# Kernel optimization log

Measured on AMD Instinct MI355X. Metric: run time of the kernel, lower is better.

The kernel has to match this reference:

```python
import jax, jax.numpy as jnp
import numpy as np

NEIGHB = 16   # k neighbors
GROUP = 32    # GroupNorm groups (== outc/2 -> per-channel instance norm)
EPS = 1e-5


def _lrelu(x, slope):
    return jnp.where(x >= 0, x, slope * x)


def _gn(x, gamma, beta, groups=GROUP, eps=EPS):
    # GroupNorm over [B, C, S, K]
    B, C, S, K = x.shape
    xr = x.reshape(B, groups, (C // groups) * S * K)
    m = xr.mean(-1, keepdims=True)
    v = xr.var(-1, keepdims=True)
    xn = ((xr - m) * jax.lax.rsqrt(v + eps)).reshape(B, C, S, K)
    return xn * gamma[None, :, None, None] + beta[None, :, None, None]


def _sample(x, rand_num, s_num, k):
    # Dynamic_sampling.forward, s_num <= P branch (s_num == P here)
    B, C, P = x.shape
    perm = jnp.argsort(rand_num, axis=1)[:, :s_num]                    # [B,S]
    sel = jnp.take_along_axis(x, perm[:, None, :], axis=2)             # [B,C,S]
    x3, s3 = x[:, :3], sel[:, :3]
    # pairwise = -||xi - qj||^2, shape [B,P,S]
    pd = -(jnp.sum(x3 * x3, 1)[:, :, None]
           - 2.0 * jnp.einsum('bcp,bcs->bps', x3, s3)
           + jnp.sum(s3 * s3, 1)[:, None, :])
    _, idx = jax.lax.top_k(pd.transpose(0, 2, 1), k)                   # [B,S,k]
    # torch: topk(dim=-2) gives [B,k,S], then .view(B,s_num,k) -> row-major
    # reinterpretation (NOT a transpose). Replicate exactly:
    idx = idx.transpose(0, 2, 1).reshape(B, s_num, k)
    xT = x.transpose(0, 2, 1)                                          # [B,P,C]
    feat = jax.vmap(lambda xt, ii: xt[ii])(xT, idx)                    # [B,S,k,C]
    return feat.transpose(0, 3, 1, 2)                                  # [B,C,S,k]


def _forward(x, rand_num, w_pe, g_pe, b_pe, w_conv, g_conv, b_conv,
             w_att1, w_att2, w_b1, w_b2, num_points):
    x1 = _sample(x, jax.lax.stop_gradient(rand_num), num_points, NEIGHB)  # [B,4,S,K]
    PA = x1[:, :3]                                                        # [B,3,S,K]
    PC = x1[:, :3, :, 0:1]                                                # [B,3,S,1]
    diff = PA - PC
    # safe sqrt: diff at K=0 is exactly 0 -> clamp to keep grads finite
    temp = jnp.sqrt(jnp.clip(jnp.sum(diff * diff, 1, keepdims=True), 1e-12))
    PEmb = jnp.concatenate([PA, jnp.broadcast_to(PC, PA.shape), diff, temp], axis=1)  # [B,10,S,K]
    PEmb = _lrelu(_gn(jnp.einsum('oc,bcsk->bosk', w_pe, PEmb), g_pe, b_pe), 0.2)
    x_ = _lrelu(_gn(jnp.einsum('oc,bcsk->bosk', w_conv, x1), g_conv, b_conv), 0.2)
    feature = jnp.concatenate([x_, PEmb], axis=1)                         # [B,64,S,K]
    att = jnp.einsum('oc,bcsk->bosk', w_att2,
                     _lrelu(jnp.einsum('oc,bcsk->bosk', w_att1, feature), 0.2))
    att = jax.nn.softmax(att, axis=-1)                                    # over K
    feature = jnp.sum(feature * att, axis=-1)                             # [B,64,S]
    Fea1 = jnp.einsum('oc,bcs->bos', w_b1, feature)
    Fea2 = jnp.einsum('oc,bcs->bos', w_b2, x1[:, :, :, 0])
    out = _lrelu(Fea1 + Fea2, 0.1)
    return jnp.concatenate([x1[:, :3, :, 0], out], axis=1)                # [B,67,S]


def setup_inputs() -> dict:
    key = jax.random.key(0)
    ks = jax.random.split(key, 10)
    B, C, P = 2, 4, 8192
    sc = 0.1
    x = jax.random.normal(ks[0], (B, C, P), jnp.float32)
    rand_num = jax.random.uniform(ks[1], (B, P), jnp.float32)
    w_pe = jax.random.normal(ks[2], (32, 10), jnp.float32) * sc
    g_pe = jnp.ones((32,), jnp.float32)
    b_pe = jnp.zeros((32,), jnp.float32)
    w_conv = jax.random.normal(ks[3], (32, 4), jnp.float32) * sc
    g_conv = jnp.ones((32,), jnp.float32)
    b_conv = jnp.zeros((32,), jnp.float32)
    w_att1 = jax.random.normal(ks[4], (32, 64), jnp.float32) * sc
    w_att2 = jax.random.normal(ks[5], (1, 32), jnp.float32) * sc
    w_b1 = jax.random.normal(ks[6], (64, 64), jnp.float32) * sc
    w_b2 = jax.random.normal(ks[7], (64, 4), jnp.float32) * sc
    return dict(x=x, rand_num=rand_num, w_pe=w_pe, g_pe=g_pe, b_pe=b_pe,
                w_conv=w_conv, g_conv=g_conv, b_conv=b_conv,
                w_att1=w_att1, w_att2=w_att2, w_b1=w_b1, w_b2=w_b2,
                num_points=8192)


def reference(x, rand_num, w_pe, g_pe, b_pe, w_conv, g_conv, b_conv,
              w_att1, w_att2, w_b1, w_b2, num_points):
    return _forward(x, rand_num, w_pe, g_pe, b_pe, w_conv, g_conv, b_conv,
                    w_att1, w_att2, w_b1, w_b2, num_points)
```

## Files before the change

### kernel.cpp

```cpp
#include <hip/hip_runtime.h>
#include <stdint.h>

#define PN 8192
#define SN 8192
#define KNB 16
#define SUBS 4
#define NCH1 8
#define CHUNK1 256
#define NCOL 4
#define COLCH (PN / NCOL)
#define SCAP 56
#define MARGIN 1.0e-3f
#define NRCH 8
#define RCH (PN / NRCH)

#define KEY_SENTINEL ((long long)0x8000000000000000ULL)
#define PD_SCALE 2199023255552.0

__device__ __forceinline__ void bitonic_sort16(float* b) {
#pragma unroll
    for (int k = 2; k <= 16; k <<= 1) {
#pragma unroll
        for (int j = k >> 1; j > 0; j >>= 1) {
#pragma unroll
            for (int i = 0; i < 16; ++i) {
                int l = i ^ j;
                if (l > i) {
                    float lo = fminf(b[i], b[l]), hi = fmaxf(b[i], b[l]);
                    bool up = ((i & k) == 0);
                    b[i] = up ? lo : hi;
                    b[l] = up ? hi : lo;
                }
            }
        }
    }
}
__device__ __forceinline__ void merge16(float* r, const float* b) {
    float t[16];
#pragma unroll
    for (int i = 0; i < 16; ++i) t[i] = fminf(r[i], b[15 - i]);
#pragma unroll
    for (int j = 8; j > 0; j >>= 1) {
#pragma unroll
        for (int i = 0; i < 16; ++i) {
            int l = i ^ j;
            if (l > i) {
                float lo = fminf(t[i], t[l]), hi = fmaxf(t[i], t[l]);
                t[i] = lo; t[l] = hi;
            }
        }
    }
#pragma unroll
    for (int i = 0; i < 16; ++i) r[i] = t[i];
}

__global__ void pack_pts_kernel(const float* __restrict__ x, float4* __restrict__ pts) {
    int i = blockIdx.x * 256 + threadIdx.x;
    int b = i >> 13, p = i & (PN - 1);
    const float* xb = x + (size_t)b * 4 * PN;
    pts[i] = make_float4(xb[p], xb[PN + p], xb[2 * PN + p], 0.f);
}

__global__ __launch_bounds__(256) void rank_count_kernel(const float* __restrict__ rnd,
        unsigned short* __restrict__ rcnt) {
    __shared__ unsigned long long lk[RCH];
    const int chunk = blockIdx.x, sg = blockIdx.y, b = blockIdx.z;
    const unsigned int* rb = (const unsigned int*)rnd + b * PN;
    const int cbase = chunk * RCH;
    for (int c = threadIdx.x; c < RCH; c += 256) {
        int j = cbase + c;
        lk[c] = ((unsigned long long)rb[j] << 13) | (unsigned)j;
    }
    __syncthreads();
    const int i = sg * 256 + threadIdx.x;
    const unsigned long long ki = ((unsigned long long)rb[i] << 13) | (unsigned)i;
    int cnt = 0;
#pragma unroll 8
    for (int c = 0; c < RCH; ++c) cnt += (lk[c] < ki) ? 1 : 0;
    rcnt[(((size_t)(b * NRCH + chunk)) << 13) + i] = (unsigned short)cnt;
}

__global__ void rank_scatter_kernel(const unsigned short* __restrict__ rcnt,
                                    int* __restrict__ perm) {
    int t = blockIdx.x * 256 + threadIdx.x;
    int b = t >> 13, i = t & (PN - 1);
    int rank = 0;
#pragma unroll
    for (int ch = 0; ch < NRCH; ++ch)
        rank += rcnt[(((size_t)(b * NRCH + ch)) << 13) + i];
    perm[b * PN + rank] = i;
}

__global__ __launch_bounds__(256) void knn_val16_kernel(const float4* __restrict__ pts,
        const int* __restrict__ perm, float* __restrict__ vv) {
    const int chunk = blockIdx.x, sg = blockIdx.y, b = blockIdx.z;
    const float4* pb = pts + b * PN;
    const int pbase = chunk * CHUNK1;
    const int s = sg * 256 + threadIdx.x;
    const float4 qp = pb[perm[b * PN + s]];
    float r[16];
#pragma unroll
    for (int i = 0; i < 16; ++i) r[i] = 3.0e38f;
    for (int t = 0; t < CHUNK1; t += 16) {
        float bv[16];
#pragma unroll
        for (int u = 0; u < 16; ++u) {
            float4 pp = pb[SUBS * (pbase + t + u)];
            float dx = qp.x - pp.x, dy = qp.y - pp.y, dz = qp.z - pp.z;
            bv[u] = dx * dx + dy * dy + dz * dz;
        }
        bitonic_sort16(bv);
        merge16(r, bv);
    }
    float* ov = vv + ((size_t)(b * NCH1 + chunk) * 16) * SN + s;
#pragma unroll
    for (int i = 0; i < 16; ++i) ov[(size_t)i * SN] = r[i];
}

__global__ void knn_thr_kernel(const float* __restrict__ vv, float* __restrict__ thrbuf) {
    int t = blockIdx.x * 256 + threadIdx.x;
    int b = t >> 13, s = t & (SN - 1);
    float r[16], bl[16];
    const float* v0 = vv + ((size_t)(b * NCH1) * 16) * SN + s;
#pragma unroll
    for (int i = 0; i < 16; ++i) r[i] = v0[(size_t)i * SN];
    for (int ch = 1; ch < NCH1; ++ch) {
        const float* vc = vv + ((size_t)(b * NCH1 + ch) * 16) * SN + s;
#pragma unroll
        for (int i = 0; i < 16; ++i) bl[i] = vc[(size_t)i * SN];
        merge16(r, bl);
    }
    thrbuf[b * SN + s] = r[15] + MARGIN;
}

#define MAKEKEY(pp, c, out) do { \
    double dx_ = qx - (double)(pp).x; \
    double dy_ = qy - (double)(pp).y; \
    double dz_ = qz - (double)(pp).z; \
    double dd_ = dx_ * dx_ + dy_ * dy_ + dz_ * dz_; \
    long long sc_ = (long long)floor(-dd_ * PD_SCALE); \
    (out) = (sc_ << 13) | (long long)(8191 - (c)); \
} while (0)

#define INS16(kkv) do { long long nk = (kkv); if (nk > k15) { \
    k15 = (nk > k14) ? k14 : ((nk > k15) ? nk : k15); \
    k14 = (nk > k13) ? k13 : ((nk > k14) ? nk : k14); \
    k13 = (nk > k12) ? k12 : ((nk > k13) ? nk : k13); \
    k12 = (nk > k11) ? k11 : ((nk > k12) ? nk : k12); \
    k11 = (nk > k10) ? k10 : ((nk > k11) ? nk : k11); \
    k10 = (nk > k9 ) ? k9  : ((nk > k10) ? nk : k10); \
    k9  = (nk > k8 ) ? k8  : ((nk > k9 ) ? nk : k9 ); \
    k8  = (nk > k7 ) ? k7  : ((nk > k8 ) ? nk : k8 ); \
    k7  = (nk > k6 ) ? k6  : ((nk > k7 ) ? nk : k7 ); \
    k6  = (nk > k5 ) ? k5  : ((nk > k6 ) ? nk : k6 ); \
    k5  = (nk > k4 ) ? k4  : ((nk > k5 ) ? nk : k5 ); \
    k4  = (nk > k3 ) ? k3  : ((nk > k4 ) ? nk : k4 ); \
    k3  = (nk > k2 ) ? k2  : ((nk > k3 ) ? nk : k3 ); \
    k2  = (nk > k1 ) ? k1  : ((nk > k2 ) ? nk : k2 ); \
    k1  = (nk > k0 ) ? k0  : ((nk > k1 ) ? nk : k1 ); \
    k0  = (nk > k0 ) ? nk  : k0; \
} } while (0)

#define QPROC(pp, cidx) do { \
    float dx_ = qp.x - (pp).x, dy_ = qp.y - (pp).y, dz_ = qp.z - (pp).z; \
    float dd_ = dx_ * dx_; dd_ += dy_ * dy_; dd_ += dz_ * dz_; \
    if (dd_ < thr) { if (cnt < SCAP) surv[cnt][tid] = (unsigned short)(cidx); ++cnt; } \
} while (0)

__global__ __launch_bounds__(256) void knn_chunk_kernel(const float4* __restrict__ pts,
        const int* __restrict__ perm, const float* __restrict__ thrbuf,
        long long* __restrict__ partK) {
    __shared__ unsigned short surv[SCAP][256];
    const int chunk = blockIdx.x, sg = blockIdx.y, b = blockIdx.z;
    const float4* pb = pts + b * PN;
    const int pbase = chunk * COLCH;
    const int tid = threadIdx.x;
    const int s = sg * 256 + tid;
    const int bs = b * SN + s;
    const float4 qp = pb[perm[bs]];
    const float thr = thrbuf[bs];
    int cnt = 0;
    const float4* cp = pb + pbase;
    float4 a0 = cp[0], a1 = cp[1], a2 = cp[2], a3 = cp[3];
    float4 a4 = cp[4], a5 = cp[5], a6 = cp[6], a7 = cp[7];
    int c = 0;
    for (; c < COLCH - 8; c += 8) {
        float4 n0 = cp[c + 8],  n1 = cp[c + 9],  n2 = cp[c + 10], n3 = cp[c + 11];
        float4 n4 = cp[c + 12], n5 = cp[c + 13], n6 = cp[c + 14], n7 = cp[c + 15];
        QPROC(a0, pbase + c + 0);
        QPROC(a1, pbase + c + 1);
        QPROC(a2, pbase + c + 2);
        QPROC(a3, pbase + c + 3);
        QPROC(a4, pbase + c + 4);
        QPROC(a5, pbase + c + 5);
        QPROC(a6, pbase + c + 6);
        QPROC(a7, pbase + c + 7);
        a0 = n0; a1 = n1; a2 = n2; a3 = n3;
        a4 = n4; a5 = n5; a6 = n6; a7 = n7;
    }
    QPROC(a0, pbase + c + 0);
    QPROC(a1, pbase + c + 1);
    QPROC(a2, pbase + c + 2);
    QPROC(a3, pbase + c + 3);
    QPROC(a4, pbase + c + 4);
    QPROC(a5, pbase + c + 5);
    QPROC(a6, pbase + c + 6);
    QPROC(a7, pbase + c + 7);
    const double qx = qp.x, qy = qp.y, qz = qp.z;
    long long k0 = KEY_SENTINEL, k1 = KEY_SENTINEL, k2 = KEY_SENTINEL, k3 = KEY_SENTINEL,
              k4 = KEY_SENTINEL, k5 = KEY_SENTINEL, k6 = KEY_SENTINEL, k7 = KEY_SENTINEL,
              k8 = KEY_SENTINEL, k9 = KEY_SENTINEL, k10 = KEY_SENTINEL, k11 = KEY_SENTINEL,
              k12 = KEY_SENTINEL, k13 = KEY_SENTINEL, k14 = KEY_SENTINEL, k15 = KEY_SENTINEL;
    if (cnt <= SCAP) {
        for (int u = 0; u < cnt; u += 4) {
            int c0i = surv[u][tid];
            int c1i = (u + 1 < cnt) ? (int)surv[u + 1][tid] : 0;
            int c2i = (u + 2 < cnt) ? (int)surv[u + 2][tid] : 0;
            int c3i = (u + 3 < cnt) ? (int)surv[u + 3][tid] : 0;
            float4 p0 = pb[c0i], p1 = pb[c1i], p2 = pb[c2i], p3 = pb[c3i];
            long long kk0, kk1, kk2, kk3;
            MAKEKEY(p0, c0i, kk0);
            MAKEKEY(p1, c1i, kk1);
            MAKEKEY(p2, c2i, kk2);
            MAKEKEY(p3, c3i, kk3);
            kk1 = (u + 1 < cnt) ? kk1 : KEY_SENTINEL;
            kk2 = (u + 2 < cnt) ? kk2 : KEY_SENTINEL;
            kk3 = (u + 3 < cnt) ? kk3 : KEY_SENTINEL;
            INS16(kk0);
            INS16(kk1);
            INS16(kk2);
            INS16(kk3);
        }
    } else {
        for (int cc = 0; cc < COLCH; ++cc) {
            float4 pp = cp[cc];
            long long kk;
            MAKEKEY(pp, pbase + cc, kk);
            INS16(kk);
        }
    }
    long long* ok = partK + ((size_t)(b * NCOL + chunk) * SN + s) * KNB;
    ok[0]  = k0;  ok[1]  = k1;  ok[2]  = k2;  ok[3]  = k3;
    ok[4]  = k4;  ok[5]  = k5;  ok[6]  = k6;  ok[7]  = k7;
    ok[8]  = k8;  ok[9]  = k9;  ok[10] = k10; ok[11] = k11;
    ok[12] = k12; ok[13] = k13; ok[14] = k14; ok[15] = k15;
}

__global__ void knn_merge_kernel(const long long* __restrict__ partK, int* __restrict__ knn) {
    int t = blockIdx.x * 64 + threadIdx.x;
    int b = t >> 13, s = t & (SN - 1);
    const long long* K0 = partK + ((size_t)(b * NCOL + 0) * SN + s) * KNB;
    const long long* K1 = partK + ((size_t)(b * NCOL + 1) * SN + s) * KNB;
    const long long* K2 = partK + ((size_t)(b * NCOL + 2) * SN + s) * KNB;
    const long long* K3 = partK + ((size_t)(b * NCOL + 3) * SN + s) * KNB;
    long long h0 = K0[0], h1 = K1[0], h2 = K2[0], h3 = K3[0];
    int p0 = 1, p1 = 1, p2 = 1, p3 = 1;
    int* ob = knn + (size_t)b * (SN * KNB);
    for (int r = 0; r < KNB; ++r) {
        long long m01 = h0 > h1 ? h0 : h1;
        long long m23 = h2 > h3 ? h2 : h3;
        long long m = m01 > m23 ? m01 : m23;
        ob[(size_t)r * SN + s] = 8191 - (int)(m & 8191);
        if (m == h0)      { h0 = (p0 < KNB) ? K0[p0] : KEY_SENTINEL; ++p0; }
        else if (m == h1) { h1 = (p1 < KNB) ? K1[p1] : KEY_SENTINEL; ++p1; }
        else if (m == h2) { h2 = (p2 < KNB) ? K2[p2] : KEY_SENTINEL; ++p2; }
        else              { h3 = (p3 < KNB) ? K3[p3] : KEY_SENTINEL; ++p3; }
    }
}

__global__ __launch_bounds__(256) void stats_kernel(const float* __restrict__ x,
        const int* __restrict__ knn, const float* __restrict__ w_pe,
        const float* __restrict__ w_conv, float* __restrict__ wavepart) {
    const int blk = blockIdx.x;
    const int b = blockIdx.y;
    const int w = threadIdx.x >> 6, l = threadIdx.x & 63;
    float wr[10];
#pragma unroll
    for (int c = 0; c < 10; ++c) wr[c] = 0.f;
    if (l < 32) {
#pragma unroll
        for (int c = 0; c < 4; ++c) wr[c] = w_conv[l * 4 + c];
    } else {
#pragma unroll
        for (int c = 0; c < 10; ++c) wr[c] = w_pe[(l - 32) * 10 + c];
    }
    const float* xb = x + (size_t)b * 4 * PN;
    const int* kb = knn + (size_t)b * (SN * KNB);
    float s1 = 0.f, s2 = 0.f;
    const int nbase = blk * 512 + w * 128;
#pragma unroll 2
    for (int it = 0; it < 128; ++it) {
        int n = nbase + it;
        int i  = kb[n];
        int i0 = kb[n & ~15];
        float xa0 = xb[i], xa1 = xb[PN + i], xa2 = xb[2 * PN + i], xa3 = xb[3 * PN + i];
        float xc0 = xb[i0], xc1 = xb[PN + i0], xc2 = xb[2 * PN + i0];
        float d0 = xa0 - xc0, d1 = xa1 - xc1, d2 = xa2 - xc2;
        float dd = d0 * d0; dd += d1 * d1; dd += d2 * d2;
        float temp = sqrtf(fmaxf(dd, 1e-12f));
        float r;
        if (l < 32) {
            r = wr[0] * xa0 + wr[1] * xa1 + wr[2] * xa2 + wr[3] * xa3;
        } else {
            r = wr[0] * xa0 + wr[1] * xa1 + wr[2] * xa2
              + wr[3] * xc0 + wr[4] * xc1 + wr[5] * xc2
              + wr[6] * d0 + wr[7] * d1 + wr[8] * d2 + wr[9] * temp;
        }
        s1 += r;
        s2 += r * r;
    }
    const int wslot = blk * 4 + w;
    wavepart[((size_t)b * 1024 + wslot) * 128 + l] = s1;
    wavepart[((size_t)b * 1024 + wslot) * 128 + 64 + l] = s2;
}

__global__ void finalize_kernel(const float* __restrict__ wavepart,
        const float* __restrict__ g_pe, const float* __restrict__ b_pe,
        const float* __restrict__ g_conv, const float* __restrict__ b_conv,
        float* __restrict__ scsh) {
    const int t = threadIdx.x;
    const int b = t >> 7, k = t & 127;
    float acc = 0.f;
    for (int w = 0; w < 1024; ++w) acc += wavepart[((size_t)b * 1024 + w) * 128 + k];
    __shared__ float sums[2][128];
    sums[b][k] = acc;
    __syncthreads();
    if (k < 64) {
        const float N = 131072.f;
        float mean = sums[b][k] / N;
        float var = sums[b][64 + k] / N - mean * mean;
        float rstd = 1.0f / sqrtf(var + 1e-5f);
        float gam = (k < 32) ? g_conv[k] : g_pe[k - 32];
        float bet = (k < 32) ? b_conv[k] : b_pe[k - 32];
        float sc = gam * rstd;
        scsh[(b * 64 + k) * 2 + 0] = sc;
        scsh[(b * 64 + k) * 2 + 1] = bet - mean * sc;
    }
}

__global__ __launch_bounds__(256) void fused_main_kernel(
        const float* __restrict__ x, const int* __restrict__ knn,
        const float* __restrict__ w_pe, const float* __restrict__ w_conv,
        const float* __restrict__ w_att1, const float* __restrict__ w_att2,
        const float* __restrict__ w_b1, const float* __restrict__ w_b2,
        const float* __restrict__ scsh, float* __restrict__ out) {
    __shared__ float wb1T[64 * 64];
    __shared__ float wb2T[4 * 64];
    for (int i = threadIdx.x; i < 64 * 64; i += 256) wb1T[(i & 63) * 64 + (i >> 6)] = w_b1[i];
    { int i = threadIdx.x; wb2T[(i & 3) * 64 + (i >> 2)] = w_b2[i]; }
    __syncthreads();
    const int gidx = blockIdx.x;
    const int b = gidx >> 9;
    const int sb = (gidx & 511) << 4;
    const int l = threadIdx.x & 63;
    const int w = threadIdx.x >> 6;
    const int g = l >> 4, j = l & 15;
    const int s = sb + (w << 2) + g;
    const int srcl = g << 4;
    const float* xb = x + (size_t)b * 4 * PN;
    const int i1 = knn[(size_t)b * (SN * KNB) + (size_t)s * KNB + j];
    float xa0 = xb[i1], xa1 = xb[PN + i1], xa2 = xb[2 * PN + i1], xa3 = xb[3 * PN + i1];
    float xc0 = __shfl(xa0, srcl), xc1 = __shfl(xa1, srcl);
    float xc2 = __shfl(xa2, srcl), xc3 = __shfl(xa3, srcl);
    float d0 = xa0 - xc0, d1 = xa1 - xc1, d2 = xa2 - xc2;
    float dd = d0 * d0; dd += d1 * d1; dd += d2 * d2;
    float temp = sqrtf(fmaxf(dd, 1e-12f));
    float pem[10] = {xa0, xa1, xa2, xc0, xc1, xc2, d0, d1, d2, temp};
    float f[64];
    const float* ssb = scsh + b * 128;
#pragma unroll
    for (int o = 0; o < 32; ++o) {
        float r = w_conv[o * 4 + 0] * xa0;
        r += w_conv[o * 4 + 1] * xa1;
        r += w_conv[o * 4 + 2] * xa2;
        r += w_conv[o * 4 + 3] * xa3;
        r = r * ssb[o * 2 + 0] + ssb[o * 2 + 1];
        f[o] = (r >= 0.f) ? r : 0.2f * r;
    }
#pragma unroll
    for (int o = 0; o < 32; ++o) {
        float r = 0.f;
#pragma unroll
        for (int c = 0; c < 10; ++c) r += w_pe[o * 10 + c] * pem[c];
        r = r * ssb[(32 + o) * 2 + 0] + ssb[(32 + o) * 2 + 1];
        f[32 + o] = (r >= 0.f) ? r : 0.2f * r;
    }
    float logit = 0.f;
#pragma unroll 2
    for (int o = 0; o < 32; ++o) {
        float a = 0.f;
#pragma unroll
        for (int c = 0; c < 64; ++c) a += w_att1[o * 64 + c] * f[c];
        a = (a >= 0.f) ? a : 0.2f * a;
        logit += w_att2[o] * a;
    }
    float mx = logit;
    mx = fmaxf(mx, __shfl_xor(mx, 1));
    mx = fmaxf(mx, __shfl_xor(mx, 2));
    mx = fmaxf(mx, __shfl_xor(mx, 4));
    mx = fmaxf(mx, __shfl_xor(mx, 8));
    float e = expf(logit - mx);
    float se = e;
    se += __shfl_xor(se, 1);
    se += __shfl_xor(se, 2);
    se += __shfl_xor(se, 4);
    se += __shfl_xor(se, 8);
    float att = e / se;
#pragma unroll
    for (int c = 0; c < 64; ++c) {
        float v = f[c] * att;
        v += __shfl_xor(v, 1);
        v += __shfl_xor(v, 2);
        v += __shfl_xor(v, 4);
        v += __shfl_xor(v, 8);
        f[c] = v;
    }
    float o0 = 0.f, o1 = 0.f, o2 = 0.f, o3 = 0.f;
#pragma unroll
    for (int c = 0; c < 64; ++c) {
        float4 wv = *reinterpret_cast<const float4*>(&wb1T[c * 64 + 4 * j]);
        o0 += wv.x * f[c]; o1 += wv.y * f[c]; o2 += wv.z * f[c]; o3 += wv.w * f[c];
    }
    {
        float4 wv = *reinterpret_cast<const float4*>(&wb2T[0 * 64 + 4 * j]);
        o0 += wv.x * xc0; o1 += wv.y * xc0; o2 += wv.z * xc0; o3 += wv.w * xc0;
        wv = *reinterpret_cast<const float4*>(&wb2T[1 * 64 + 4 * j]);
        o0 += wv.x * xc1; o1 += wv.y * xc1; o2 += wv.z * xc1; o3 += wv.w * xc1;
        wv = *reinterpret_cast<const float4*>(&wb2T[2 * 64 + 4 * j]);
        o0 += wv.x * xc2; o1 += wv.y * xc2; o2 += wv.z * xc2; o3 += wv.w * xc2;
        wv = *reinterpret_cast<const float4*>(&wb2T[3 * 64 + 4 * j]);
        o0 += wv.x * xc3; o1 += wv.y * xc3; o2 += wv.z * xc3; o3 += wv.w * xc3;
    }
    o0 = (o0 >= 0.f) ? o0 : 0.1f * o0;
    o1 = (o1 >= 0.f) ? o1 : 0.1f * o1;
    o2 = (o2 >= 0.f) ? o2 : 0.1f * o2;
    o3 = (o3 >= 0.f) ? o3 : 0.1f * o3;
    float* ob = out + (size_t)b * 67 * SN;
    const int oc = 3 + 4 * j;
    ob[(size_t)(oc + 0) * SN + s] = o0;
    ob[(size_t)(oc + 1) * SN + s] = o1;
    ob[(size_t)(oc + 2) * SN + s] = o2;
    ob[(size_t)(oc + 3) * SN + s] = o3;
    if (j < 3) ob[(size_t)j * SN + s] = (j == 0) ? xc0 : ((j == 1) ? xc1 : xc2);
}

extern "C" void kernel_launch(void* const* d_in, const int* in_sizes, int n_in,
                              void* d_out, int out_size, void* d_ws, size_t ws_size,
                              hipStream_t stream) {
    (void)in_sizes; (void)n_in; (void)out_size; (void)ws_size;
    const float* x      = (const float*)d_in[0];
    const float* rnd    = (const float*)d_in[1];
    const float* w_pe   = (const float*)d_in[2];
    const float* g_pe   = (const float*)d_in[3];
    const float* b_pe   = (const float*)d_in[4];
    const float* w_conv = (const float*)d_in[5];
    const float* g_conv = (const float*)d_in[6];
    const float* b_conv = (const float*)d_in[7];
    const float* w_att1 = (const float*)d_in[8];
    const float* w_att2 = (const float*)d_in[9];
    const float* w_b1   = (const float*)d_in[10];
    const float* w_b2   = (const float*)d_in[11];
    float* out = (float*)d_out;
    char* ws = (char*)d_ws;
    float4*         pts    = (float4*)        (ws + 0);
    int*            perm   = (int*)           (ws + 262144);
    unsigned short* rcnt   = (unsigned short*)(ws + 327680);
    float*          vv     = (float*)         (ws + 327680);
    long long*      partK  = (long long*)     (ws + 327680);
    float*          wavept = (float*)         (ws + 327680);
    float*          thrbuf = (float*)         (ws + 8716288);
    int*            knn    = (int*)           (ws + 9043968);
    float*          scsh   = (float*)         (ws + 10092544);

    pack_pts_kernel<<<64, 256, 0, stream>>>(x, pts);
    rank_count_kernel<<<dim3(NRCH, 32, 2), 256, 0, stream>>>(rnd, rcnt);
    rank_scatter_kernel<<<64, 256, 0, stream>>>(rcnt, perm);
    knn_val16_kernel<<<dim3(NCH1, 32, 2), 256, 0, stream>>>(pts, perm, vv);
    knn_thr_kernel<<<64, 256, 0, stream>>>(vv, thrbuf);
    knn_chunk_kernel<<<dim3(NCOL, 32, 2), 256, 0, stream>>>(pts, perm, thrbuf, partK);
    knn_merge_kernel<<<256, 64, 0, stream>>>(partK, knn);
    stats_kernel<<<dim3(256, 2), 256, 0, stream>>>(x, knn, w_pe, w_conv, wavept);
    finalize_kernel<<<1, 256, 0, stream>>>(wavept, g_pe, b_pe, g_conv, b_conv, scsh);
    fused_main_kernel<<<1024, 256, 0, stream>>>(x, knn, w_pe, w_conv, w_att1, w_att2,
                                                w_b1, w_b2, scsh, out);
}
```

Baseline: 351.0 us.

## Split KNN scan into 8 chunks with in-block pairwise top-16 merge

The KNN candidate scan now splits the points into 8 chunks instead of 4. Each 256-thread block covers 128 queries, and its two halves scan adjacent chunks. The second half writes its top-16 keys to shared memory, and the first half merges them with an insertion pass, so the global partial-key layout and the merge kernel still see 4 lists. This doubles the grid size to raise parallelism and halve the per-thread scan length, and lowers the survivor capacity to 32 to fit the extra shared buffer. The cost is a block barrier plus a serial 16-key merge, and more queries may hit the capacity fallback path.

After: 307.2 us. 12.5% less time.

```diff
diff --git a/kernel.cpp b/kernel.cpp
--- a/kernel.cpp
+++ b/kernel.cpp
@@ -7,9 +7,10 @@
 #define SUBS 4
 #define NCH1 8
 #define CHUNK1 256
-#define NCOL 4
-#define COLCH (PN / NCOL)
-#define SCAP 56
+#define NSCAN 8
+#define SCANCH (PN / NSCAN)
+#define NPAIR 4
+#define SCAP 32
 #define MARGIN 1.0e-3f
 #define NRCH 8
 #define RCH (PN / NRCH)
@@ -167,16 +168,20 @@
     if (dd_ < thr) { if (cnt < SCAP) surv[cnt][tid] = (unsigned short)(cidx); ++cnt; } \
 } while (0)
 
-__global__ __launch_bounds__(256) void knn_chunk_kernel(const float4* __restrict__ pts,
+__global__ __launch_bounds__(256) void knn_pair_kernel(const float4* __restrict__ pts,
         const int* __restrict__ perm, const float* __restrict__ thrbuf,
         long long* __restrict__ partK) {
     __shared__ unsigned short surv[SCAP][256];
-    const int chunk = blockIdx.x, sg = blockIdx.y, b = blockIdx.z;
+    __shared__ long long kbuf[128][17];
+    const int pair = blockIdx.x, sg = blockIdx.y, b = blockIdx.z;
+    const int tid = threadIdx.x;
+    const int half = tid >> 7;
+    const int lane = tid & 127;
+    const int s = sg * 128 + lane;
+    const int bs = b * SN + s;
     const float4* pb = pts + b * PN;
-    const int pbase = chunk * COLCH;
-    const int tid = threadIdx.x;
-    const int s = sg * 256 + tid;
-    const int bs = b * SN + s;
+    const int chunk = 2 * pair + half;
+    const int pbase = chunk * SCANCH;
     const float4 qp = pb[perm[bs]];
     const float thr = thrbuf[bs];
     int cnt = 0;
@@ -184,7 +189,7 @@
     float4 a0 = cp[0], a1 = cp[1], a2 = cp[2], a3 = cp[3];
     float4 a4 = cp[4], a5 = cp[5], a6 = cp[6], a7 = cp[7];
     int c = 0;
-    for (; c < COLCH - 8; c += 8) {
+    for (; c < SCANCH - 8; c += 8) {
         float4 n0 = cp[c + 8],  n1 = cp[c + 9],  n2 = cp[c + 10], n3 = cp[c + 11];
         float4 n4 = cp[c + 12], n5 = cp[c + 13], n6 = cp[c + 14], n7 = cp[c + 15];
         QPROC(a0, pbase + c + 0);
@@ -232,27 +237,38 @@
             INS16(kk3);
         }
     } else {
-        for (int cc = 0; cc < COLCH; ++cc) {
+        for (int cc = 0; cc < SCANCH; ++cc) {
             float4 pp = cp[cc];
             long long kk;
             MAKEKEY(pp, pbase + cc, kk);
             INS16(kk);
         }
     }
-    long long* ok = partK + ((size_t)(b * NCOL + chunk) * SN + s) * KNB;
-    ok[0]  = k0;  ok[1]  = k1;  ok[2]  = k2;  ok[3]  = k3;
-    ok[4]  = k4;  ok[5]  = k5;  ok[6]  = k6;  ok[7]  = k7;
-    ok[8]  = k8;  ok[9]  = k9;  ok[10] = k10; ok[11] = k11;
-    ok[12] = k12; ok[13] = k13; ok[14] = k14; ok[15] = k15;
+    if (half) {
+        kbuf[lane][0]  = k0;  kbuf[lane][1]  = k1;  kbuf[lane][2]  = k2;  kbuf[lane][3]  = k3;
+        kbuf[lane][4]  = k4;  kbuf[lane][5]  = k5;  kbuf[lane][6]  = k6;  kbuf[lane][7]  = k7;
+        kbuf[lane][8]  = k8;  kbuf[lane][9]  = k9;  kbuf[lane][10] = k10; kbuf[lane][11] = k11;
+        kbuf[lane][12] = k12; kbuf[lane][13] = k13; kbuf[lane][14] = k14; kbuf[lane][15] = k15;
+    }
+    __syncthreads();
+    if (!half) {
+#pragma unroll
+        for (int r = 0; r < 16; ++r) INS16(kbuf[lane][r]);
+        long long* ok = partK + ((size_t)(b * NPAIR + pair) * SN + s) * KNB;
+        ok[0]  = k0;  ok[1]  = k1;  ok[2]  = k2;  ok[3]  = k3;
+        ok[4]  = k4;  ok[5]  = k5;  ok[6]  = k6;  ok[7]  = k7;
+        ok[8]  = k8;  ok[9]  = k9;  ok[10] = k10; ok[11] = k11;
+        ok[12] = k12; ok[13] = k13; ok[14] = k14; ok[15] = k15;
+    }
 }
 
 __global__ void knn_merge_kernel(const long long* __restrict__ partK, int* __restrict__ knn) {
     int t = blockIdx.x * 64 + threadIdx.x;
     int b = t >> 13, s = t & (SN - 1);
-    const long long* K0 = partK + ((size_t)(b * NCOL + 0) * SN + s) * KNB;
-    const long long* K1 = partK + ((size_t)(b * NCOL + 1) * SN + s) * KNB;
-    const long long* K2 = partK + ((size_t)(b * NCOL + 2) * SN + s) * KNB;
-    const long long* K3 = partK + ((size_t)(b * NCOL + 3) * SN + s) * KNB;
+    const long long* K0 = partK + ((size_t)(b * NPAIR + 0) * SN + s) * KNB;
+    const long long* K1 = partK + ((size_t)(b * NPAIR + 1) * SN + s) * KNB;
+    const long long* K2 = partK + ((size_t)(b * NPAIR + 2) * SN + s) * KNB;
+    const long long* K3 = partK + ((size_t)(b * NPAIR + 3) * SN + s) * KNB;
     long long h0 = K0[0], h1 = K1[0], h2 = K2[0], h3 = K3[0];
     int p0 = 1, p1 = 1, p2 = 1, p3 = 1;
     int* ob = knn + (size_t)b * (SN * KNB);
@@ -477,7 +493,7 @@
     rank_scatter_kernel<<<64, 256, 0, stream>>>(rcnt, perm);
     knn_val16_kernel<<<dim3(NCH1, 32, 2), 256, 0, stream>>>(pts, perm, vv);
     knn_thr_kernel<<<64, 256, 0, stream>>>(vv, thrbuf);
-    knn_chunk_kernel<<<dim3(NCOL, 32, 2), 256, 0, stream>>>(pts, perm, thrbuf, partK);
+    knn_pair_kernel<<<dim3(NPAIR, 64, 2), 256, 0, stream>>>(pts, perm, thrbuf, partK);
     knn_merge_kernel<<<256, 64, 0, stream>>>(partK, knn);
     stats_kernel<<<dim3(256, 2), 256, 0, stream>>>(x, knn, w_pe, w_conv, wavept);
     finalize_kernel<<<1, 256, 0, stream>>>(wavept, g_pe, b_pe, g_conv, b_conv, scsh);
```
